# Performance work log

Hardware: AMD Instinct MI355X
Metric: run time of the kernel (lower is better)

The kernel has to match this reference:

```python
import jax, jax.numpy as jnp
import numpy as np


def conv1d(x, w, b):
    # x: (N, Cin, W), w: (Cout, Cin, K) -> (N, Cout, W-K+1), VALID conv (torch Conv1d)
    y = jax.lax.conv_general_dilated(x, w, (1,), 'VALID', dimension_numbers=('NCH', 'OIH', 'NCH'))
    return y + b[None, :, None]


def cnn_block(x, w, b):
    # conv1d then MaxPool1d over the full valid length -> (N, Cout)
    return jnp.max(conv1d(x, w, b), axis=2)


def highway(x, Wp, bp, Wg, bg):
    p = jax.nn.relu(x @ Wp.T + bp)
    g = jax.nn.sigmoid(x @ Wg.T + bg)
    return g * p + (1.0 - g) * x


def lstm_masked(x, lens, Wih, Whh, bih, bhh):
    # x: (N, Wt, E); lens: (N,) valid lengths. Emulates pack_padded_sequence +
    # nn.LSTM + pad_packed_sequence: outputs are h_t for t < len, zeros after.
    N, Wt, _ = x.shape
    H = Whh.shape[1]
    bias = bih + bhh
    h0 = jnp.zeros((N, H), x.dtype)

    def step(carry, inp):
        xt, t = inp
        h, c = carry
        z = xt @ Wih.T + h @ Whh.T + bias  # (N, 4H), gate order i,f,g,o
        i, f, g, o = jnp.split(z, 4, axis=-1)
        c2 = jax.nn.sigmoid(f) * c + jax.nn.sigmoid(i) * jnp.tanh(g)
        h2 = jax.nn.sigmoid(o) * jnp.tanh(c2)
        valid = (t < lens)[:, None]
        h2 = jnp.where(valid, h2, h)
        c2 = jnp.where(valid, c2, c)
        return (h2, c2), jnp.where(valid, h2, jnp.zeros_like(h2))

    xs = jnp.moveaxis(x, 1, 0)  # (Wt, N, E)
    ts = jnp.arange(Wt)
    _, out = jax.lax.scan(step, (h0, h0), (xs, ts))
    return jnp.moveaxis(out, 0, 1)  # (N, Wt, H)


def setup_inputs() -> dict:
    key = jax.random.key(0)
    ks = jax.random.split(key, 32)
    B, T = 32, 48
    WL, WA, WE = 33, 50, 30
    EL, EA, EE, H = 300, 988, 20, 128
    CL, CA, CE = 128, 256, 64
    s = 0.02
    inp = {
        'x_lin': jax.random.normal(ks[0], (B, T, WL, EL), jnp.float32),
        'x_aco': jax.random.normal(ks[1], (B, T, WA, EA), jnp.float32),
        'x_emo': jax.random.normal(ks[2], (B, T, WE, EE), jnp.float32),
        'window_length': jax.random.randint(ks[3], (B, T), 0, WE).astype(jnp.int32) + 1,
        'length': jax.random.randint(ks[4], (B,), 1, T + 1).astype(jnp.int32),
        # CNN params
        'convL_w': s * jax.random.normal(ks[5], (CL, EL, 5), jnp.float32),
        'convL_b': jnp.zeros((CL,), jnp.float32),
        'convA_w': s * jax.random.normal(ks[6], (CA, EA, 10), jnp.float32),
        'convA_b': jnp.zeros((CA,), jnp.float32),
        'convE_w': s * jax.random.normal(ks[7], (CE, H, 3), jnp.float32),
        'convE_b': jnp.zeros((CE,), jnp.float32),
        # Highway params
        'hwL_Wp': s * jax.random.normal(ks[8], (CL, CL), jnp.float32),
        'hwL_bp': jnp.zeros((CL,), jnp.float32),
        'hwL_Wg': s * jax.random.normal(ks[9], (CL, CL), jnp.float32),
        'hwL_bg': jnp.zeros((CL,), jnp.float32),
        'hwA_Wp': s * jax.random.normal(ks[10], (CA, CA), jnp.float32),
        'hwA_bp': jnp.zeros((CA,), jnp.float32),
        'hwA_Wg': s * jax.random.normal(ks[11], (CA, CA), jnp.float32),
        'hwA_bg': jnp.zeros((CA,), jnp.float32),
        'hwE_Wp': s * jax.random.normal(ks[12], (CE, CE), jnp.float32),
        'hwE_bp': jnp.zeros((CE,), jnp.float32),
        'hwE_Wg': s * jax.random.normal(ks[13], (CE, CE), jnp.float32),
        'hwE_bg': jnp.zeros((CE,), jnp.float32),
        # LSTM params (nn.LSTM, 1 layer, batch_first)
        'lstm_Wih': s * jax.random.normal(ks[14], (4 * H, EE), jnp.float32),
        'lstm_Whh': s * jax.random.normal(ks[15], (4 * H, H), jnp.float32),
        'lstm_bih': jnp.zeros((4 * H,), jnp.float32),
        'lstm_bhh': jnp.zeros((4 * H,), jnp.float32),
    }
    return inp


def reference(x_lin, x_aco, x_emo, window_length, length,
              convL_w, convL_b, convA_w, convA_b, convE_w, convE_b,
              hwL_Wp, hwL_bp, hwL_Wg, hwL_bg,
              hwA_Wp, hwA_bp, hwA_Wg, hwA_bg,
              hwE_Wp, hwE_bp, hwE_Wg, hwE_bg,
              lstm_Wih, lstm_Whh, lstm_bih, lstm_bhh):
    B, T = x_lin.shape[:2]
    # Linguistic: per-window CNN + Highway (dropout = identity in eval)
    xl = x_lin.reshape(B * T, x_lin.shape[2], x_lin.shape[3]).transpose(0, 2, 1)  # (BT, 300, WL)
    outL = highway(cnn_block(xl, convL_w, convL_b), hwL_Wp, hwL_bp, hwL_Wg, hwL_bg)
    outL = outL.reshape(B, T, -1)
    # Acoustic
    xa = x_aco.reshape(B * T, x_aco.shape[2], x_aco.shape[3]).transpose(0, 2, 1)  # (BT, 988, WA)
    outA = highway(cnn_block(xa, convA_w, convA_b), hwA_Wp, hwA_bp, hwA_Wg, hwA_bg)
    outA = outA.reshape(B, T, -1)
    # Emotient: ragged per-window LSTM (packed semantics) -> CNN -> Highway
    xe = x_emo.reshape(B * T, x_emo.shape[2], x_emo.shape[3])  # (BT, WE, 20)
    lens = window_length.reshape(B * T)
    h = lstm_masked(xe, lens, lstm_Wih, lstm_Whh, lstm_bih, lstm_bhh)  # (BT, WE, 128)
    outE = highway(cnn_block(h.transpose(0, 2, 1), convE_w, convE_b), hwE_Wp, hwE_bp, hwE_Wg, hwE_bg)
    outE = outE.reshape(B, T, -1)
    # Concatenate modalities -> (B, T, 128+256+64) fed to the downstream head
    return jnp.concatenate([outL, outA, outE], axis=2)
```

## Files before the change

### kernel.cpp

```cpp
#include <hip/hip_runtime.h>
#include <hip/hip_bf16.h>
#include <math.h>

#define BTOT 1536
#define EL 300
#define ELP 320
#define WL_ 33
#define CL 128
#define LOUTL 29
#define KPL 1600
#define EA 988
#define EAP 992
#define WA_ 50
#define CA 256
#define LOUTA 41
#define KPA 9920
#define EE 20
#define WE_ 30
#define HH 128
#define CE 64
#define LOUTE 28
#define KPE 384
#define KDIML 1500
#define KDIMA 9880
#define KDIME 384

typedef __attribute__((ext_vector_type(4))) float f32x4;
typedef __attribute__((ext_vector_type(8))) short short8;

__device__ __forceinline__ unsigned short f2bf(float f) {
    unsigned int x = __float_as_uint(f);
    unsigned int r = (x + 0x7fffu + ((x >> 16) & 1u)) >> 16;
    return (unsigned short)r;
}

__device__ __forceinline__ float sigmf(float x) {
    return __builtin_amdgcn_rcpf(1.f + __expf(-x));
}
__device__ __forceinline__ float tanh_fast(float x) {
    return 1.f - 2.f * __builtin_amdgcn_rcpf(1.f + __expf(2.f * x));
}

#define GLD16(gp, lp) __builtin_amdgcn_global_load_lds( \
    (const __attribute__((address_space(1))) void*)(gp), \
    (__attribute__((address_space(3))) void*)(lp), 16, 0, 0)

template<int N> __device__ __forceinline__ void vmwait() {
    if constexpr (N == 0) asm volatile("s_waitcnt vmcnt(0)" ::: "memory");
    else if constexpr (N == 1) asm volatile("s_waitcnt vmcnt(1)" ::: "memory");
    else if constexpr (N == 2) asm volatile("s_waitcnt vmcnt(2)" ::: "memory");
    else if constexpr (N == 3) asm volatile("s_waitcnt vmcnt(3)" ::: "memory");
    else if constexpr (N == 4) asm volatile("s_waitcnt vmcnt(4)" ::: "memory");
    else if constexpr (N == 5) asm volatile("s_waitcnt vmcnt(5)" ::: "memory");
    else if constexpr (N == 6) asm volatile("s_waitcnt vmcnt(6)" ::: "memory");
    else if constexpr (N == 8) asm volatile("s_waitcnt vmcnt(8)" ::: "memory");
    else static_assert(N == 0, "add case");
}

__device__ __forceinline__ void tr_one(const float* a, float* at, int R, int C, int idx) {
    int r = idx / C, c = idx - r * C;
    at[c * R + r] = a[idx];
}
template<int CIN, int CINP, int KW, int COUT, int KPAD>
__device__ __forceinline__ void wt_one(const float* w, unsigned short* wt, int idx) {
    int co = idx / KPAD;
    int p  = idx - co * KPAD;
    int k  = p / CINP;
    int c  = p - k * CINP;
    float v = 0.f;
    if (k < KW && c < CIN) v = w[(co * CIN + c) * KW + k];
    wt[idx] = f2bf(v);
}
template<bool BIG>
__global__ void prep_all(const float* hwL_Wp, float* WpTL, const float* hwL_Wg, float* WgTL,
                         const float* hwA_Wp, float* WpTA, const float* hwA_Wg, float* WgTA,
                         const float* hwE_Wp, float* WpTE, const float* hwE_Wg, float* WgTE,
                         const float* lstm_Wih, float* WihT, const float* lstm_Whh, float* WhhT,
                         const float* convL_w, unsigned short* wtL,
                         const float* convE_w, unsigned short* wtE,
                         const float* convA_w, unsigned short* wtA,
                         unsigned short* whh_bf, unsigned short* wihp_bf) {
    constexpr int S1 = 16384, S2 = 16384, S3 = 65536, S4 = 65536, S5 = 4096, S6 = 4096;
    constexpr int S7 = 512 * 20, S8 = 512 * 128;
    constexpr int S9 = 128 * KPL, S10 = 64 * KPE, S11 = 512 * 128, S12 = 512 * 32;
    constexpr int S13 = CA * KPA;
    constexpr int SMALL = S1 + S2 + S3 + S4 + S5 + S6 + S7 + S8;
    constexpr int TOTAL = BIG ? (SMALL + S9 + S10 + S11 + S12 + S13) : SMALL;
    int stride = gridDim.x * blockDim.x;
    for (int i = blockIdx.x * blockDim.x + threadIdx.x; i < TOTAL; i += stride) {
        int idx = i;
        if (idx < S1) { tr_one(hwL_Wp, WpTL, 128, 128, idx); continue; } idx -= S1;
        if (idx < S2) { tr_one(hwL_Wg, WgTL, 128, 128, idx); continue; } idx -= S2;
        if (idx < S3) { tr_one(hwA_Wp, WpTA, 256, 256, idx); continue; } idx -= S3;
        if (idx < S4) { tr_one(hwA_Wg, WgTA, 256, 256, idx); continue; } idx -= S4;
        if (idx < S5) { tr_one(hwE_Wp, WpTE, 64, 64, idx); continue; } idx -= S5;
        if (idx < S6) { tr_one(hwE_Wg, WgTE, 64, 64, idx); continue; } idx -= S6;
        if (idx < S7) { tr_one(lstm_Wih, WihT, 512, 20, idx); continue; } idx -= S7;
        if (idx < S8) { tr_one(lstm_Whh, WhhT, 512, 128, idx); continue; } idx -= S8;
        if constexpr (BIG) {
            if (idx < S9) { wt_one<EL, ELP, 5, CL, KPL>(convL_w, wtL, idx); continue; } idx -= S9;
            if (idx < S10) { wt_one<HH, HH, 3, CE, KPE>(convE_w, wtE, idx); continue; } idx -= S10;
            if (idx < S11) { whh_bf[idx] = f2bf(lstm_Whh[idx]); continue; } idx -= S11;
            if (idx < S12) { int col = idx >> 5, e = idx & 31;
                             wihp_bf[idx] = (e < 20) ? f2bf(lstm_Wih[col * 20 + e]) : (unsigned short)0;
                             continue; } idx -= S12;
            wt_one<EA, EAP, 10, CA, KPA>(convA_w, wtA, idx);
        }
    }
}

template<int CIN, int CINP>
__device__ __forceinline__ void cvt_chunk(const float* in, unsigned short* out, int idx) {
    constexpr int CH = CINP / 8;
    int row = idx / CH, c0 = (idx - row * CH) * 8;
    const float* src = in + (size_t)row * CIN + c0;
    union { short8 s; unsigned short u[8]; } o;
    if (c0 + 8 <= CIN) {
        float4 v0 = *(const float4*)src;
        float4 v1 = *(const float4*)(src + 4);
        o.u[0]=f2bf(v0.x); o.u[1]=f2bf(v0.y); o.u[2]=f2bf(v0.z); o.u[3]=f2bf(v0.w);
        o.u[4]=f2bf(v1.x); o.u[5]=f2bf(v1.y); o.u[6]=f2bf(v1.z); o.u[7]=f2bf(v1.w);
    } else {
        #pragma unroll
        for (int j = 0; j < 8; ++j) o.u[j] = (c0 + j < CIN) ? f2bf(src[j]) : (unsigned short)0;
    }
    *(short8*)(out + (size_t)row * CINP + c0) = o.s;
}

#define LSTM_BLOCKS 96
#define CVTA_BLOCKS 1440

__global__ __launch_bounds__(512, 1)
void lstm_cvt(const float* __restrict__ x_emo,
              const unsigned short* __restrict__ wihp_bf, const unsigned short* __restrict__ whh_bf,
              const float* __restrict__ bih, const float* __restrict__ bhh,
              const int* __restrict__ lens, unsigned short* __restrict__ hbuf,
              const float* __restrict__ xa, unsigned short* __restrict__ outa)
{
    __shared__ __align__(16) unsigned short xq[WE_ * 16 * 32];
    __shared__ __align__(16) char h_s[2 * 16 * HH * 2];

    if (blockIdx.x >= LSTM_BLOCKS) {
        constexpr int NAC = (BTOT * WA_) * (EAP / 8);
        int stride = CVTA_BLOCKS * 512;
        for (int i = (blockIdx.x - LSTM_BLOCKS) * 512 + threadIdx.x; i < NAC; i += stride)
            cvt_chunk<EA, EAP>(xa, outa, i);
        return;
    }

    const int tid  = threadIdx.x;
    const int w    = tid >> 6;
    const int lane = tid & 63;
    const int lr   = lane & 15;
    const int lq   = lane >> 4;
    const int s0   = blockIdx.x * 16;
    const int c    = w * 16 + lr;

    short8 bfr[4][4];
    short8 bw[4];
    float bj[4];
    #pragma unroll
    for (int g = 0; g < 4; ++g) {
        int col = g * 128 + c;
        #pragma unroll
        for (int kt = 0; kt < 4; ++kt)
            bfr[g][kt] = *(const short8*)(whh_bf + (size_t)col * 128 + kt * 32 + lq * 8);
        bw[g] = *(const short8*)(wihp_bf + (size_t)col * 32 + lq * 8);
        bj[g] = bih[col] + bhh[col];
    }
    int len4[4];
    #pragma unroll
    for (int j = 0; j < 4; ++j) len4[j] = lens[s0 + lq * 4 + j];

    for (int i = tid; i < WE_ * 16 * 32; i += 512) {
        int t = i >> 9, r = (i >> 5) & 15, e = i & 31;
        xq[i] = (e < 20) ? f2bf(x_emo[(((size_t)(s0 + r) * WE_) + t) * 20 + e]) : (unsigned short)0;
    }
    for (int i = tid; i < 2048; i += 512) ((unsigned int*)h_s)[i] = 0u;

    float c_prev[4] = {0.f, 0.f, 0.f, 0.f};
    unsigned short hb_prev[4] = {0, 0, 0, 0};
    __syncthreads();

    for (int t = 0; t < WE_; ++t) {
        const char* hsr = h_s + (t & 1) * 4096;
        char* hsw = h_s + ((t & 1) ^ 1) * 4096;
        short8 ax = *(const short8*)((const char*)xq + (size_t)(t * 16 + lr) * 64 + lq * 16);
        short8 af[4];
        #pragma unroll
        for (int kt = 0; kt < 4; ++kt)
            af[kt] = *(const short8*)(hsr + ((lr * 256 + kt * 64 + lq * 16) ^ ((lr & 7) << 4)));
        f32x4 acc[4];
        #pragma unroll
        for (int g = 0; g < 4; ++g)
            acc[g] = __builtin_amdgcn_mfma_f32_16x16x32_bf16(ax, bw[g], (f32x4){0.f,0.f,0.f,0.f}, 0, 0, 0);
        #pragma unroll
        for (int kt = 0; kt < 4; ++kt)
            #pragma unroll
            for (int g = 0; g < 4; ++g)
                acc[g] = __builtin_amdgcn_mfma_f32_16x16x32_bf16(af[kt], bfr[g][kt], acc[g], 0, 0, 0);
        #pragma unroll
        for (int j = 0; j < 4; ++j) {
            int s = lq * 4 + j;
            float zi = acc[0][j] + bj[0];
            float zf = acc[1][j] + bj[1];
            float zg = acc[2][j] + bj[2];
            float zo = acc[3][j] + bj[3];
            float si = sigmf(zi), sf = sigmf(zf), so = sigmf(zo);
            float tg = tanh_fast(zg);
            float c2 = sf * c_prev[j] + si * tg;
            float h2 = so * tanh_fast(c2);
            bool valid = (t < len4[j]);
            c_prev[j] = valid ? c2 : c_prev[j];
            unsigned short h2b = f2bf(h2);
            unsigned short hn = valid ? h2b : hb_prev[j];
            hb_prev[j] = hn;
            *(unsigned short*)(hsw + (((s * HH + c) * 2) ^ ((s & 7) << 4))) = hn;
            hbuf[(((size_t)(s0 + s) * WE_) + t) * HH + c] = valid ? h2b : (unsigned short)0;
        }
        __syncthreads();
    }
}

#define CONVA_BLOCKS 768
#define CVTL_BLOCKS 512
__global__ __launch_bounds__(256, 2)
void conv_a_v11(const unsigned short* __restrict__ xb, const unsigned short* __restrict__ wt,
                const float* __restrict__ bias, float* __restrict__ pooled,
                const float* __restrict__ xl, unsigned short* __restrict__ outl)
{
    constexpr int LOUT = LOUTA, WIN = WA_, CINP = EAP, BN = 128, COUT = CA;
    constexpr int CCH  = CINP / 32;
    constexpr int KB   = CINP * 2;
    constexpr int KTOTB = CINP * 10 * 2;
    constexpr int ABUF = 4 * 64 * 64;
    constexpr int BBUF = BN * 64;
    constexpr int CPQ  = 96;

    __shared__ __align__(16) char smem[2 * ABUF + 5 * BBUF];

    if (blockIdx.x >= CONVA_BLOCKS) {
        constexpr int NLC = (BTOT * WL_) * (ELP / 8);
        int stride = CVTL_BLOCKS * 256;
        for (int i = (blockIdx.x - CONVA_BLOCKS) * 256 + threadIdx.x; i < NLC; i += stride)
            cvt_chunk<EL, ELP>(xl, outl, i);
        return;
    }

    const int tid  = threadIdx.x;
    const int lane = tid & 63;
    const int wid  = tid >> 6;
    const int lr   = lane & 15;
    const int lq   = lane >> 4;
    const int lq16 = lq * 16;

    int xcd = blockIdx.x & 7;
    int n = xcd & 1;
    int m = (xcd >> 1) * CPQ + (blockIdx.x >> 3);

    f32x4 acc[3][8];
    #pragma unroll
    for (int i = 0; i < 3; ++i)
        #pragma unroll
        for (int j = 0; j < 8; ++j) acc[i][j] = (f32x4){0.f, 0.f, 0.f, 0.f};

    const int aw_r = tid >> 2;
    const int aw   = (aw_r < WIN) ? aw_r : (WIN - 1);
    const int slot = tid & 3;
    const char* asrc[4];
    #pragma unroll
    for (int i = 0; i < 4; ++i)
        asrc[i] = (const char*)xb + ((size_t)((m * 4 + i) * WIN + aw)) * KB
                + ((slot * 16) ^ (((aw_r >> 1) & 3) << 4));
    const char* bsrc[2];
    #pragma unroll
    for (int i = 0; i < 2; ++i) {
        int col = (tid + i * 256) >> 2;
        bsrc[i] = (const char*)wt + (size_t)(n * BN + col) * KTOTB
                + ((slot * 16) ^ (((col >> 1) & 3) << 4));
    }

    char* const abuf0 = smem;
    char* const abuf1 = smem + ABUF;
    char* const bbase = smem + 2 * ABUF;

    int cbo[8];
    #pragma unroll
    for (int nf = 0; nf < 8; ++nf) {
        int cb = nf * 16 + lr;
        cbo[nf] = cb * 64 + (lq16 ^ (((cb >> 1) & 3) << 4));
    }

    #pragma unroll
    for (int i = 0; i < 4; ++i)
        GLD16(asrc[i], abuf0 + i * 4096 + tid * 16);
    #pragma unroll
    for (int s = 0; s < 3; ++s) {
        GLD16(bsrc[0] + s * KB, bbase + s * BBUF + tid * 16);
        GLD16(bsrc[1] + s * KB, bbase + s * BBUF + 4096 + tid * 16);
    }
    vmwait<0>();
    __builtin_amdgcn_s_barrier();

    int bcur = 0;

#define VSTEP(KK, DOA, DOBAR, WN, DOBSTG, CHN) do {                                \
    const char* bb = bbase + bcur * BBUF;                                          \
    short8 afr[3];                                                                 \
    _Pragma("unroll")                                                              \
    for (int o = 0; o < 3; ++o) {                                                  \
        int row = o * 16 + lr + (KK);                                              \
        afr[o] = *(const short8*)(awave + row * 64 + (lq16 ^ (((row >> 1) & 3) << 4))); \
    }                                                                              \
    short8 bf[8];                                                                  \
    _Pragma("unroll")                                                              \
    for (int nf = 0; nf < 8; ++nf) bf[nf] = *(const short8*)(bb + cbo[nf]);        \
    if (DOBSTG) {                                                                  \
        constexpr int K3 = ((KK) + 3 < 10) ? (KK) + 3 : (KK) - 7;                  \
        int boff = K3 * KB + (CHN) * 64;                                           \
        int b3 = bcur + 3; if (b3 >= 5) b3 -= 5;                                   \
        char* bstg = bbase + b3 * BBUF;                                            \
        GLD16(bsrc[0] + boff, bstg + tid * 16);                                    \
        GLD16(bsrc[1] + boff, bstg + 4096 + tid * 16);                             \
    }                                                                              \
    if (DOA) GLD16(asrc[(KK) - 5] + (size_t)(ci + 1) * 64,                         \
                   abn + ((KK) - 5) * 4096 + tid * 16);                            \
    __builtin_amdgcn_s_setprio(1);                                                 \
    _Pragma("unroll")                                                              \
    for (int nf = 0; nf < 8; ++nf)                                                 \
        _Pragma("unroll")                                                          \
        for (int o = 0; o < 3; ++o)                                                \
            acc[o][nf] = __builtin_amdgcn_mfma_f32_16x16x32_bf16(afr[o], bf[nf], acc[o][nf], 0, 0, 0); \
    __builtin_amdgcn_s_setprio(0);                                                 \
    if (DOBAR) { vmwait<WN>(); asm volatile("" ::: "memory");                      \
                 __builtin_amdgcn_s_barrier(); }                                   \
    bcur = (bcur == 4) ? 0 : bcur + 1;                                             \
} while (0)

    for (int ci = 0; ci < CCH - 1; ++ci) {
        const char* ab = (ci & 1) ? abuf1 : abuf0;
        char* abn = (ci & 1) ? abuf0 : abuf1;
        const char* awave = ab + wid * 4096;
        VSTEP(0, false, false, 0, true, ci);
        VSTEP(1, false, true,  2, true, ci);
        VSTEP(2, false, false, 0, true, ci);
        VSTEP(3, false, true,  2, true, ci);
        VSTEP(4, false, false, 0, true, ci);
        VSTEP(5, true,  true,  3, true, ci);
        VSTEP(6, true,  false, 0, true, ci);
        VSTEP(7, true,  true,  3, true, ci + 1);
        VSTEP(8, true,  false, 0, true, ci + 1);
        VSTEP(9, false, true,  2, true, ci + 1);
    }
    {
        const int ci = CCH - 1;
        const char* ab = (ci & 1) ? abuf1 : abuf0;
        char* abn = (ci & 1) ? abuf0 : abuf1; (void)abn;
        const char* awave = ab + wid * 4096;
        VSTEP(0, false, false, 0, true,  ci);
        VSTEP(1, false, true,  2, true,  ci);
        VSTEP(2, false, false, 0, true,  ci);
        VSTEP(3, false, true,  2, true,  ci);
        VSTEP(4, false, false, 0, true,  ci);
        VSTEP(5, false, true,  2, true,  ci);
        VSTEP(6, false, false, 0, true,  ci);
        VSTEP(7, false, true,  0, false, ci);
        VSTEP(8, false, false, 0, false, ci);
        VSTEP(9, false, true,  0, false, ci);
    }
#undef VSTEP

    const int bt = m * 4 + wid;
    #pragma unroll
    for (int nf = 0; nf < 8; ++nf) {
        float mx = -INFINITY;
        #pragma unroll
        for (int o = 0; o < 3; ++o) {
            int rb = o * 16 + lq * 4;
            #pragma unroll
            for (int j = 0; j < 4; ++j)
                if (rb + j < LOUT) mx = fmaxf(mx, acc[o][nf][j]);
        }
        mx = fmaxf(mx, __shfl_xor(mx, 16, 64));
        mx = fmaxf(mx, __shfl_xor(mx, 32, 64));
        if (lane < 16) {
            int col = n * BN + nf * 16 + lane;
            pooled[(size_t)bt * COUT + col] = mx + bias[col];
        }
    }
}

template<int LOUT, int WIN, int CINP, int KW, int BN, int NS, int MFR, int COUT>
__global__ __launch_bounds__(256, 2)
void conv_pool_v10(const unsigned short* __restrict__ xb, const unsigned short* __restrict__ wt,
                   const float* __restrict__ bias, float* __restrict__ pooled)
{
    constexpr int CCH   = CINP / 32;
    constexpr int KB    = CINP * 2;
    constexpr int KTOTB = CINP * KW * 2;
    constexpr int NFR   = BN / 16;
    constexpr int B_IT  = BN / 64;
    constexpr int ABUF  = 4 * 64 * 64;
    constexpr int BBUF  = BN * 64;
    constexpr int CPQ   = (BTOT / 4) / 4;

    __shared__ __align__(16) char smem[2 * ABUF + 4 * BBUF];

    const int tid  = threadIdx.x;
    const int lane = tid & 63;
    const int wid  = tid >> 6;
    const int lr   = lane & 15;
    const int lq   = lane >> 4;
    const int lq16 = lq * 16;

    int m, n;
    if constexpr (NS == 2) {
        int xcd = blockIdx.x & 7;
        n = xcd & 1;
        m = (xcd >> 1) * CPQ + (blockIdx.x >> 3);
    } else {
        m = blockIdx.x; n = 0;
    }

    f32x4 acc[MFR][NFR];
    #pragma unroll
    for (int i = 0; i < MFR; ++i)
        #pragma unroll
        for (int j = 0; j < NFR; ++j) acc[i][j] = (f32x4){0.f, 0.f, 0.f, 0.f};

    const int aw_r = tid >> 2;
    const int aw   = (aw_r < WIN) ? aw_r : (WIN - 1);
    const int slot = tid & 3;
    const char* asrc[4];
    #pragma unroll
    for (int i = 0; i < 4; ++i)
        asrc[i] = (const char*)xb + ((size_t)((m * 4 + i) * WIN + aw)) * KB
                + ((slot * 16) ^ (((aw_r >> 1) & 3) << 4));
    const char* bsrc[B_IT];
    #pragma unroll
    for (int i = 0; i < B_IT; ++i) {
        int col = (tid + i * 256) >> 2;
        bsrc[i] = (const char*)wt + (size_t)(n * BN + col) * KTOTB
                + ((slot * 16) ^ (((col >> 1) & 3) << 4));
    }

    char* const abuf0 = smem;
    char* const abuf1 = smem + ABUF;
    char* const bbase = smem + 2 * ABUF;

    int cbo[NFR];
    #pragma unroll
    for (int nf = 0; nf < NFR; ++nf) {
        int cb = nf * 16 + lr;
        cbo[nf] = cb * 64 + (lq16 ^ (((cb >> 1) & 3) << 4));
    }

    #pragma unroll
    for (int i = 0; i < 4; ++i)
        GLD16(asrc[i], abuf0 + i * 4096 + tid * 16);
    #pragma unroll
    for (int s = 0; s < 3; ++s)
        #pragma unroll
        for (int i = 0; i < B_IT; ++i)
            GLD16(bsrc[i] + s * KB, bbase + s * BBUF + i * 4096 + tid * 16);
    vmwait<0>();
    __builtin_amdgcn_s_barrier();

    int bcur = 0;

#define STEP(KK, WN, TAIL) do {                                                    \
    const char* bb = bbase + bcur * BBUF;                                          \
    short8 afr[MFR];                                                               \
    _Pragma("unroll")                                                              \
    for (int o = 0; o < MFR; ++o) {                                                \
        int row = o * 16 + lr + (KK);                                              \
        afr[o] = *(const short8*)(awave + row * 64 + (lq16 ^ (((row >> 1) & 3) << 4))); \
    }                                                                              \
    short8 bf[NFR];                                                                \
    _Pragma("unroll")                                                              \
    for (int nf = 0; nf < NFR; ++nf) bf[nf] = *(const short8*)(bb + cbo[nf]);      \
    if (!(TAIL) || (KK) < KW - 3) {                                                \
        constexpr int k3_ = ((KK) + 3 < KW) ? (KK) + 3 : (KK) + 3 - KW;            \
        int boff = k3_ * KB + (((KK) + 3 < KW) ? ci : ci + 1) * 64;                \
        char* bstg = bbase + ((bcur + 3) & 3) * BBUF;                              \
        _Pragma("unroll")                                                          \
        for (int i = 0; i < B_IT; ++i)                                             \
            GLD16(bsrc[i] + boff, bstg + i * 4096 + tid * 16);                     \
    }                                                                              \
    if (!(TAIL)) {                                                                 \
        if (KW >= 8) {                                                             \
            if ((KK) < 4)                                                          \
                GLD16(asrc[(KK) & 3] + (size_t)(ci + 1) * 64, abn + ((KK) & 3) * 4096 + tid * 16); \
        } else if ((KK) == 0) {                                                    \
            _Pragma("unroll")                                                      \
            for (int i = 0; i < 4; ++i)                                            \
                GLD16(asrc[i] + (size_t)(ci + 1) * 64, abn + i * 4096 + tid * 16); \
        }                                                                          \
    }                                                                              \
    __builtin_amdgcn_s_setprio(1);                                                 \
    _Pragma("unroll")                                                              \
    for (int nf = 0; nf < NFR; ++nf)                                               \
        _Pragma("unroll")                                                          \
        for (int o = 0; o < MFR; ++o)                                              \
            acc[o][nf] = __builtin_amdgcn_mfma_f32_16x16x32_bf16(afr[o], bf[nf], acc[o][nf], 0, 0, 0); \
    __builtin_amdgcn_s_setprio(0);                                                 \
    vmwait<WN>();                                                                  \
    asm volatile("" ::: "memory");                                                 \
    __builtin_amdgcn_s_barrier();                                                  \
    bcur = (bcur + 1) & 3;                                                         \
} while (0)

    for (int ci = 0; ci < CCH - 1; ++ci) {
        const char* ab = (ci & 1) ? abuf1 : abuf0;
        char* abn = (ci & 1) ? abuf0 : abuf1;
        const char* awave = ab + wid * 4096;
        if constexpr (KW == 5) {
            STEP(0, 8, false); STEP(1, 8, false); STEP(2, 4, false); STEP(3, 4, false); STEP(4, 4, false);
        } else {
            STEP(0, 6, false); STEP(1, 6, false); STEP(2, 2, false);
        }
    }
    {
        const int ci = CCH - 1;
        const char* ab = (ci & 1) ? abuf1 : abuf0;
        char* abn = (ci & 1) ? abuf0 : abuf1; (void)abn;
        const char* awave = ab + wid * 4096;
        if constexpr (KW == 5) {
            STEP(0, 4, true); STEP(1, 4, true); STEP(2, 2, true); STEP(3, 0, true); STEP(4, 0, true);
        } else {
            STEP(0, 1, true); STEP(1, 0, true); STEP(2, 0, true);
        }
    }
#undef STEP

    const int bt = m * 4 + wid;
    #pragma unroll
    for (int nf = 0; nf < NFR; ++nf) {
        float mx = -INFINITY;
        #pragma unroll
        for (int o = 0; o < MFR; ++o) {
            int rb = o * 16 + lq * 4;
            #pragma unroll
            for (int j = 0; j < 4; ++j)
                if (rb + j < LOUT) mx = fmaxf(mx, acc[o][nf][j]);
        }
        mx = fmaxf(mx, __shfl_xor(mx, 16, 64));
        mx = fmaxf(mx, __shfl_xor(mx, 32, 64));
        if (lane < 16) {
            int col = n * BN + nf * 16 + lane;
            pooled[(size_t)bt * COUT + col] = mx + bias[col];
        }
    }
}

#define HWA_BLOCKS 192
#define HWL_BLOCKS 96
#define HWE_BLOCKS 48
__global__ __launch_bounds__(256)
void highway_v2(const float* __restrict__ pL, const float* __restrict__ pA, const float* __restrict__ pE,
                const float* __restrict__ WpTL, const float* __restrict__ bpL,
                const float* __restrict__ WgTL, const float* __restrict__ bgL,
                const float* __restrict__ WpTA, const float* __restrict__ bpA,
                const float* __restrict__ WgTA, const float* __restrict__ bgA,
                const float* __restrict__ WpTE, const float* __restrict__ bpE,
                const float* __restrict__ WgTE, const float* __restrict__ bgE,
                float* __restrict__ out) {
    __shared__ float xs[2048];
    int bx = blockIdx.x;
    int tid = threadIdx.x;
    if (bx < HWA_BLOCKS) {
        int bt0 = bx * 8;
        #pragma unroll
        for (int s = 0; s < 8; ++s) xs[s * 256 + tid] = pA[(size_t)(bt0 + s) * 256 + tid];
        __syncthreads();
        float p[8], g[8];
        #pragma unroll
        for (int s = 0; s < 8; ++s) { p[s] = bpA[tid]; g[s] = bgA[tid]; }
        for (int c = 0; c < 256; ++c) {
            float wp = WpTA[c * 256 + tid], wg = WgTA[c * 256 + tid];
            #pragma unroll
            for (int s = 0; s < 8; ++s) {
                float xv = xs[s * 256 + c];
                p[s] += xv * wp; g[s] += xv * wg;
            }
        }
        #pragma unroll
        for (int s = 0; s < 8; ++s) {
            float pp = fmaxf(p[s], 0.f);
            float gg = sigmf(g[s]);
            out[(size_t)(bt0 + s) * 448 + 128 + tid] = gg * pp + (1.f - gg) * xs[s * 256 + tid];
        }
    } else if (bx < HWA_BLOCKS + HWL_BLOCKS) {
        int bt0 = (bx - HWA_BLOCKS) * 16;
        for (int i = tid; i < 16 * 128; i += 256) xs[i] = pL[(size_t)bt0 * 128 + i];
        __syncthreads();
        int j = tid & 127, h = tid >> 7;
        float p[8], g[8];
        #pragma unroll
        for (int s = 0; s < 8; ++s) { p[s] = bpL[j]; g[s] = bgL[j]; }
        for (int c = 0; c < 128; ++c) {
            float wp = WpTL[c * 128 + j], wg = WgTL[c * 128 + j];
            #pragma unroll
            for (int s = 0; s < 8; ++s) {
                float xv = xs[(h * 8 + s) * 128 + c];
                p[s] += xv * wp; g[s] += xv * wg;
            }
        }
        #pragma unroll
        for (int s = 0; s < 8; ++s) {
            float pp = fmaxf(p[s], 0.f);
            float gg = sigmf(g[s]);
            out[(size_t)(bt0 + h * 8 + s) * 448 + j] = gg * pp + (1.f - gg) * xs[(h * 8 + s) * 128 + j];
        }
    } else {
        int bt0 = (bx - HWA_BLOCKS - HWL_BLOCKS) * 32;
        for (int i = tid; i < 32 * 64; i += 256) xs[i] = pE[(size_t)bt0 * 64 + i];
        __syncthreads();
        int j = tid & 63, grp = tid >> 6;
        float p[8], g[8];
        #pragma unroll
        for (int s = 0; s < 8; ++s) { p[s] = bpE[j]; g[s] = bgE[j]; }
        for (int c = 0; c < 64; ++c) {
            float wp = WpTE[c * 64 + j], wg = WgTE[c * 64 + j];
            #pragma unroll
            for (int s = 0; s < 8; ++s) {
                float xv = xs[(grp * 8 + s) * 64 + c];
                p[s] += xv * wp; g[s] += xv * wg;
            }
        }
        #pragma unroll
        for (int s = 0; s < 8; ++s) {
            float pp = fmaxf(p[s], 0.f);
            float gg = sigmf(g[s]);
            out[(size_t)(bt0 + grp * 8 + s) * 448 + 384 + j] = gg * pp + (1.f - gg) * xs[(grp * 8 + s) * 64 + j];
        }
    }
}

__global__ __launch_bounds__(512)
void lstm_kernel_f32(const float* __restrict__ x, const int* __restrict__ lens,
                     const float* __restrict__ WihT, const float* __restrict__ WhhT,
                     const float* __restrict__ bih, const float* __restrict__ bhh,
                     float* __restrict__ hout) {
    int bt = blockIdx.x;
    int j  = threadIdx.x;
    __shared__ float xs[WE_][EE];
    __shared__ __align__(16) float hs[HH];
    __shared__ float zs[512];
    for (int idx = j; idx < WE_ * EE; idx += 512)
        ((float*)xs)[idx] = x[(size_t)bt * WE_ * EE + idx];
    if (j < HH) hs[j] = 0.f;
    float wih[EE];
    #pragma unroll
    for (int e = 0; e < EE; ++e) wih[e] = WihT[e * 512 + j];
    float whh[HH];
    #pragma unroll
    for (int h = 0; h < HH; ++h) whh[h] = WhhT[h * 512 + j];
    float bjv = bih[j] + bhh[j];
    float c_reg = 0.f;
    int len = lens[bt];
    __syncthreads();
    for (int t = 0; t < WE_; ++t) {
        float z = bjv;
        #pragma unroll
        for (int e = 0; e < EE; ++e) z += wih[e] * xs[t][e];
        const float4* h4 = (const float4*)hs;
        #pragma unroll
        for (int q = 0; q < HH / 4; ++q) {
            float4 hv = h4[q];
            z += whh[4*q+0] * hv.x + whh[4*q+1] * hv.y
               + whh[4*q+2] * hv.z + whh[4*q+3] * hv.w;
        }
        zs[j] = z;
        __syncthreads();
        if (j < HH) {
            float zi = zs[j], zf = zs[HH + j], zg = zs[2*HH + j], zo = zs[3*HH + j];
            float si = 1.f / (1.f + expf(-zi));
            float sf = 1.f / (1.f + expf(-zf));
            float so = 1.f / (1.f + expf(-zo));
            float tg = tanhf(zg);
            float c2 = sf * c_reg + si * tg;
            float h2 = so * tanhf(c2);
            bool valid = (t < len);
            float hn = valid ? h2 : hs[j];
            c_reg    = valid ? c2 : c_reg;
            hout[((size_t)bt * WE_ + t) * HH + j] = valid ? h2 : 0.f;
            hs[j] = hn;
        }
        __syncthreads();
    }
}

template<int CIN, int WIN, int COUT, int KDIM, int LOUT>
__global__ __launch_bounds__(256)
void conv_pool_simple(const float* __restrict__ x, const float* __restrict__ w,
                      const float* __restrict__ bias, float* __restrict__ pooled)
{
    constexpr int KW = KDIM / CIN;
    int bt = blockIdx.x;
    int co = blockIdx.y * 64 + (threadIdx.x & 63);
    int seg = threadIdx.x >> 6;
    __shared__ float part[4][64];
    float m = -INFINITY;
    for (int l = seg; l < LOUT; l += 4) {
        float acc = 0.f;
        for (int k = 0; k < KW; ++k) {
            const float* xr = x + ((size_t)bt * WIN + l + k) * CIN;
            const float* wr = w + ((size_t)co * CIN) * KW + k;
            for (int cc = 0; cc < CIN; ++cc) acc += xr[cc] * wr[(size_t)cc * KW];
        }
        m = fmaxf(m, acc);
    }
    part[seg][threadIdx.x & 63] = m;
    __syncthreads();
    if (threadIdx.x < 64) {
        float mm = fmaxf(fmaxf(part[0][threadIdx.x], part[1][threadIdx.x]),
                         fmaxf(part[2][threadIdx.x], part[3][threadIdx.x]));
        pooled[(size_t)bt * COUT + co] = mm + bias[co];
    }
}

static inline int cdiv(int a, int b) { return (a + b - 1) / b; }

extern "C" void kernel_launch(void* const* d_in, const int* in_sizes, int n_in,
                              void* d_out, int out_size, void* d_ws, size_t ws_size,
                              hipStream_t stream) {
    const float* x_lin  = (const float*)d_in[0];
    const float* x_aco  = (const float*)d_in[1];
    const float* x_emo  = (const float*)d_in[2];
    const int*   wlen   = (const int*)  d_in[3];
    const float* convL_w = (const float*)d_in[5];
    const float* convL_b = (const float*)d_in[6];
    const float* convA_w = (const float*)d_in[7];
    const float* convA_b = (const float*)d_in[8];
    const float* convE_w = (const float*)d_in[9];
    const float* convE_b = (const float*)d_in[10];
    const float* hwL_Wp = (const float*)d_in[11];
    const float* hwL_bp = (const float*)d_in[12];
    const float* hwL_Wg = (const float*)d_in[13];
    const float* hwL_bg = (const float*)d_in[14];
    const float* hwA_Wp = (const float*)d_in[15];
    const float* hwA_bp = (const float*)d_in[16];
    const float* hwA_Wg = (const float*)d_in[17];
    const float* hwA_bg = (const float*)d_in[18];
    const float* hwE_Wp = (const float*)d_in[19];
    const float* hwE_bp = (const float*)d_in[20];
    const float* hwE_Wg = (const float*)d_in[21];
    const float* hwE_bg = (const float*)d_in[22];
    const float* lstm_Wih = (const float*)d_in[23];
    const float* lstm_Whh = (const float*)d_in[24];
    const float* lstm_bih = (const float*)d_in[25];
    const float* lstm_bhh = (const float*)d_in[26];
    float* out = (float*)d_out;

    char* p0 = (char*)d_ws;
    char* p = p0;
    auto alloc = [&](size_t bytes) { char* r = p; p += (bytes + 255) & ~(size_t)255; return r; };
    float* WpTL = (float*)alloc((size_t)CL * CL * 4);
    float* WgTL = (float*)alloc((size_t)CL * CL * 4);
    float* WpTA = (float*)alloc((size_t)CA * CA * 4);
    float* WgTA = (float*)alloc((size_t)CA * CA * 4);
    float* WpTE = (float*)alloc((size_t)CE * CE * 4);
    float* WgTE = (float*)alloc((size_t)CE * CE * 4);
    float* WihT = (float*)alloc((size_t)EE * 512 * 4);
    float* WhhT = (float*)alloc((size_t)HH * 512 * 4);
    unsigned short* whh_bf  = (unsigned short*)alloc((size_t)512 * 128 * 2);
    unsigned short* wihp_bf = (unsigned short*)alloc((size_t)512 * 32 * 2);
    void*  hbuf = (void*)alloc((size_t)BTOT * WE_ * HH * 4);
    float* pL   = (float*)alloc((size_t)BTOT * CL * 4);
    float* pA   = (float*)alloc((size_t)BTOT * CA * 4);
    float* pE   = (float*)alloc((size_t)BTOT * CE * 4);
    unsigned short* wtA = (unsigned short*)alloc((size_t)CA * KPA * 2);
    unsigned short* wtL = (unsigned short*)alloc((size_t)CL * KPL * 2);
    unsigned short* wtE = (unsigned short*)alloc((size_t)CE * KPE * 2);
    unsigned short* xlin_p = (unsigned short*)alloc((size_t)BTOT * WL_ * ELP * 2 + 64);
    unsigned short* xaco_p = (unsigned short*)alloc((size_t)BTOT * WA_ * EAP * 2 + 64);
    size_t need = (size_t)(p - p0);
    bool big = ws_size >= need;

    if (big) {
        prep_all<true><<<2048, 256, 0, stream>>>(hwL_Wp, WpTL, hwL_Wg, WgTL, hwA_Wp, WpTA, hwA_Wg, WgTA,
                                                 hwE_Wp, WpTE, hwE_Wg, WgTE, lstm_Wih, WihT, lstm_Whh, WhhT,
                                                 convL_w, wtL, convE_w, wtE, convA_w, wtA, whh_bf, wihp_bf);
        lstm_cvt<<<LSTM_BLOCKS + CVTA_BLOCKS, 512, 0, stream>>>(
            x_emo, wihp_bf, whh_bf, lstm_bih, lstm_bhh, wlen, (unsigned short*)hbuf,
            x_aco, xaco_p);
        conv_a_v11<<<CONVA_BLOCKS + CVTL_BLOCKS, 256, 0, stream>>>(
            xaco_p, wtA, convA_b, pA, x_lin, xlin_p);
        conv_pool_v10<LOUTL, WL_, ELP, 5, 128, 1, 2, CL>
            <<<384, 256, 0, stream>>>(xlin_p, wtL, convL_b, pL);
        conv_pool_v10<LOUTE, WE_, HH, 3, 64, 1, 2, CE>
            <<<384, 256, 0, stream>>>((const unsigned short*)hbuf, wtE, convE_b, pE);
        highway_v2<<<HWA_BLOCKS + HWL_BLOCKS + HWE_BLOCKS, 256, 0, stream>>>(
            pL, pA, pE, WpTL, hwL_bp, WgTL, hwL_bg, WpTA, hwA_bp, WgTA, hwA_bg,
            WpTE, hwE_bp, WgTE, hwE_bg, out);
    } else {
        prep_all<false><<<2048, 256, 0, stream>>>(hwL_Wp, WpTL, hwL_Wg, WgTL, hwA_Wp, WpTA, hwA_Wg, WgTA,
                                                  hwE_Wp, WpTE, hwE_Wg, WgTE, lstm_Wih, WihT, lstm_Whh, WhhT,
                                                  convL_w, wtL, convE_w, wtE, convA_w, wtA, whh_bf, wihp_bf);
        lstm_kernel_f32<<<BTOT, 512, 0, stream>>>(x_emo, wlen, WihT, WhhT, lstm_bih, lstm_bhh, (float*)hbuf);
        conv_pool_simple<EA, WA_, CA, KDIMA, LOUTA>
            <<<dim3(BTOT, CA / 64), 256, 0, stream>>>(x_aco, convA_w, convA_b, pA);
        conv_pool_simple<EL, WL_, CL, KDIML, LOUTL>
            <<<dim3(BTOT, CL / 64), 256, 0, stream>>>(x_lin, convL_w, convL_b, pL);
        conv_pool_simple<HH, WE_, CE, KDIME, LOUTE>
            <<<dim3(BTOT, CE / 64), 256, 0, stream>>>((const float*)hbuf, convE_w, convE_b, pE);
        highway_v2<<<HWA_BLOCKS + HWL_BLOCKS + HWE_BLOCKS, 256, 0, stream>>>(
            pL, pA, pE, WpTL, hwL_bp, WgTL, hwL_bg, WpTA, hwA_bp, WgTA, hwA_bg,
            WpTE, hwE_bp, WgTE, hwE_bg, out);
    }
}
```

Baseline: 518.6 us.

## Enlarge acoustic conv tile to 12 windows per block and merge input conversions

The acoustic conv kernel now runs 768-thread blocks covering 12 windows each, so every staged weight tile is reused by 12 waves instead of 4. Only 8 waves stage B, and the B ring shrinks from 5 to 4 buffers with a barrier on every step. The linguistic fp32-to-bf16 conversion moves out of the conv launch and into the LSTM/convert launch, which leaves the conv kernel purely compute. Costs: a larger LDS footprint (about 128KB per block), more frequent barriers, and the conversion work now sharing a launch with the LSTM.

Result: slower. 869.8 us (+67.7%).

```diff
diff --git a/kernel.cpp b/kernel.cpp
--- a/kernel.cpp
+++ b/kernel.cpp
@@ -128,23 +128,27 @@
 }
 
 #define LSTM_BLOCKS 96
-#define CVTA_BLOCKS 1440
+#define CVT_BLOCKS 1952
 
 __global__ __launch_bounds__(512, 1)
 void lstm_cvt(const float* __restrict__ x_emo,
               const unsigned short* __restrict__ wihp_bf, const unsigned short* __restrict__ whh_bf,
               const float* __restrict__ bih, const float* __restrict__ bhh,
               const int* __restrict__ lens, unsigned short* __restrict__ hbuf,
-              const float* __restrict__ xa, unsigned short* __restrict__ outa)
+              const float* __restrict__ xa, const float* __restrict__ xl,
+              unsigned short* __restrict__ outa, unsigned short* __restrict__ outl)
 {
     __shared__ __align__(16) unsigned short xq[WE_ * 16 * 32];
     __shared__ __align__(16) char h_s[2 * 16 * HH * 2];
 
     if (blockIdx.x >= LSTM_BLOCKS) {
         constexpr int NAC = (BTOT * WA_) * (EAP / 8);
-        int stride = CVTA_BLOCKS * 512;
-        for (int i = (blockIdx.x - LSTM_BLOCKS) * 512 + threadIdx.x; i < NAC; i += stride)
-            cvt_chunk<EA, EAP>(xa, outa, i);
+        constexpr int NLC = (BTOT * WL_) * (ELP / 8);
+        int stride = CVT_BLOCKS * 512;
+        for (int i = (blockIdx.x - LSTM_BLOCKS) * 512 + threadIdx.x; i < NAC + NLC; i += stride) {
+            if (i < NAC) cvt_chunk<EA, EAP>(xa, outa, i);
+            else         cvt_chunk<EL, ELP>(xl, outl, i - NAC);
+        }
         return;
     }
 
@@ -222,30 +226,19 @@
     }
 }
 
-#define CONVA_BLOCKS 768
-#define CVTL_BLOCKS 512
-__global__ __launch_bounds__(256, 2)
-void conv_a_v11(const unsigned short* __restrict__ xb, const unsigned short* __restrict__ wt,
-                const float* __restrict__ bias, float* __restrict__ pooled,
-                const float* __restrict__ xl, unsigned short* __restrict__ outl)
+#define CONVA12_BLOCKS 256
+__global__ __launch_bounds__(768, 3)
+void conv_a12(const unsigned short* __restrict__ xb, const unsigned short* __restrict__ wt,
+              const float* __restrict__ bias, float* __restrict__ pooled)
 {
-    constexpr int LOUT = LOUTA, WIN = WA_, CINP = EAP, BN = 128, COUT = CA;
+    constexpr int CINP = EAP, BN = 128, COUT = CA, KW = 10, LOUT = LOUTA, WIN = WA_;
     constexpr int CCH  = CINP / 32;
     constexpr int KB   = CINP * 2;
-    constexpr int KTOTB = CINP * 10 * 2;
-    constexpr int ABUF = 4 * 64 * 64;
+    constexpr int KTOTB = CINP * KW * 2;
+    constexpr int ABUF = 12 * 4096;
     constexpr int BBUF = BN * 64;
-    constexpr int CPQ  = 96;
-
-    __shared__ __align__(16) char smem[2 * ABUF + 5 * BBUF];
-
-    if (blockIdx.x >= CONVA_BLOCKS) {
-        constexpr int NLC = (BTOT * WL_) * (ELP / 8);
-        int stride = CVTL_BLOCKS * 256;
-        for (int i = (blockIdx.x - CONVA_BLOCKS) * 256 + threadIdx.x; i < NLC; i += stride)
-            cvt_chunk<EL, ELP>(xl, outl, i);
-        return;
-    }
+
+    __shared__ __align__(16) char smem[2 * ABUF + 4 * BBUF];
 
     const int tid  = threadIdx.x;
     const int lane = tid & 63;
@@ -253,10 +246,11 @@
     const int lr   = lane & 15;
     const int lq   = lane >> 4;
     const int lq16 = lq * 16;
+    const bool bstager = (wid < 8);
 
     int xcd = blockIdx.x & 7;
     int n = xcd & 1;
-    int m = (xcd >> 1) * CPQ + (blockIdx.x >> 3);
+    int m = (xcd >> 1) * 32 + (blockIdx.x >> 3);
 
     f32x4 acc[3][8];
     #pragma unroll
@@ -264,21 +258,18 @@
         #pragma unroll
         for (int j = 0; j < 8; ++j) acc[i][j] = (f32x4){0.f, 0.f, 0.f, 0.f};
 
-    const int aw_r = tid >> 2;
-    const int aw   = (aw_r < WIN) ? aw_r : (WIN - 1);
-    const int slot = tid & 3;
     const char* asrc[4];
     #pragma unroll
-    for (int i = 0; i < 4; ++i)
-        asrc[i] = (const char*)xb + ((size_t)((m * 4 + i) * WIN + aw)) * KB
-                + ((slot * 16) ^ (((aw_r >> 1) & 3) << 4));
-    const char* bsrc[2];
-    #pragma unroll
-    for (int i = 0; i < 2; ++i) {
-        int col = (tid + i * 256) >> 2;
-        bsrc[i] = (const char*)wt + (size_t)(n * BN + col) * KTOTB
-                + ((slot * 16) ^ (((col >> 1) & 3) << 4));
-    }
+    for (int i = 0; i < 4; ++i) {
+        int c = tid + i * 768;
+        int s = c >> 8, r = (c >> 2) & 63, slot = c & 3;
+        int rv = (r < WIN) ? r : (WIN - 1);
+        asrc[i] = (const char*)xb + ((size_t)((m * 12 + s) * WIN + rv)) * KB
+                + ((slot * 16) ^ (((r >> 1) & 3) << 4));
+    }
+    const char* bsrc = (const char*)wt
+        + (size_t)(n * BN + (tid >> 2)) * KTOTB
+        + (((tid & 3) * 16) ^ ((((tid >> 2) >> 1) & 3) << 4));
 
     char* const abuf0 = smem;
     char* const abuf1 = smem + ABUF;
@@ -293,18 +284,18 @@
 
     #pragma unroll
     for (int i = 0; i < 4; ++i)
-        GLD16(asrc[i], abuf0 + i * 4096 + tid * 16);
-    #pragma unroll
-    for (int s = 0; s < 3; ++s) {
-        GLD16(bsrc[0] + s * KB, bbase + s * BBUF + tid * 16);
-        GLD16(bsrc[1] + s * KB, bbase + s * BBUF + 4096 + tid * 16);
+        GLD16(asrc[i], abuf0 + (tid + i * 768) * 16);
+    if (bstager) {
+        #pragma unroll
+        for (int s = 0; s < 3; ++s)
+            GLD16(bsrc + s * KB, bbase + s * BBUF + tid * 16);
     }
     vmwait<0>();
     __builtin_amdgcn_s_barrier();
 
     int bcur = 0;
 
-#define VSTEP(KK, DOA, DOBAR, WN, DOBSTG, CHN) do {                                \
+#define STEP(KK, W07, W811, TAIL) do {                                             \
     const char* bb = bbase + bcur * BBUF;                                          \
     short8 afr[3];                                                                 \
     _Pragma("unroll")                                                              \
@@ -315,16 +306,13 @@
     short8 bf[8];                                                                  \
     _Pragma("unroll")                                                              \
     for (int nf = 0; nf < 8; ++nf) bf[nf] = *(const short8*)(bb + cbo[nf]);        \
-    if (DOBSTG) {                                                                  \
-        constexpr int K3 = ((KK) + 3 < 10) ? (KK) + 3 : (KK) - 7;                  \
-        int boff = K3 * KB + (CHN) * 64;                                           \
-        int b3 = bcur + 3; if (b3 >= 5) b3 -= 5;                                   \
-        char* bstg = bbase + b3 * BBUF;                                            \
-        GLD16(bsrc[0] + boff, bstg + tid * 16);                                    \
-        GLD16(bsrc[1] + boff, bstg + 4096 + tid * 16);                             \
+    if ((!(TAIL) || (KK) < KW - 3) && bstager) {                \
+        constexpr int K3 = ((KK) + 3 < KW) ? (KK) + 3 : (KK) + 3 - KW;             \
+        int boff = K3 * KB + (((KK) + 3 < KW) ? ci : ci + 1) * 64;                 \
+        GLD16(bsrc + boff, bbase + ((bcur + 3) & 3) * BBUF + tid * 16);            \
     }                                                                              \
-    if (DOA) GLD16(asrc[(KK) - 5] + (size_t)(ci + 1) * 64,                         \
-                   abn + ((KK) - 5) * 4096 + tid * 16);                            \
+    if (!(TAIL) && (KK) < 4)                  \
+        GLD16(asrc[KK] + (size_t)(ci + 1) * 64, abn + (tid + (KK) * 768) * 16);    \
     __builtin_amdgcn_s_setprio(1);                                                 \
     _Pragma("unroll")                                                              \
     for (int nf = 0; nf < 8; ++nf)                                                 \
@@ -332,45 +320,34 @@
         for (int o = 0; o < 3; ++o)                                                \
             acc[o][nf] = __builtin_amdgcn_mfma_f32_16x16x32_bf16(afr[o], bf[nf], acc[o][nf], 0, 0, 0); \
     __builtin_amdgcn_s_setprio(0);                                                 \
-    if (DOBAR) { vmwait<WN>(); asm volatile("" ::: "memory");                      \
-                 __builtin_amdgcn_s_barrier(); }                                   \
-    bcur = (bcur == 4) ? 0 : bcur + 1;                                             \
+    if (bstager) vmwait<W07>(); else vmwait<W811>();                               \
+    asm volatile("" ::: "memory");                                                 \
+    __builtin_amdgcn_s_barrier();                                                  \
+    bcur = (bcur + 1) & 3;                                                         \
 } while (0)
 
     for (int ci = 0; ci < CCH - 1; ++ci) {
         const char* ab = (ci & 1) ? abuf1 : abuf0;
         char* abn = (ci & 1) ? abuf0 : abuf1;
         const char* awave = ab + wid * 4096;
-        VSTEP(0, false, false, 0, true, ci);
-        VSTEP(1, false, true,  2, true, ci);
-        VSTEP(2, false, false, 0, true, ci);
-        VSTEP(3, false, true,  2, true, ci);
-        VSTEP(4, false, false, 0, true, ci);
-        VSTEP(5, true,  true,  3, true, ci);
-        VSTEP(6, true,  false, 0, true, ci);
-        VSTEP(7, true,  true,  3, true, ci + 1);
-        VSTEP(8, true,  false, 0, true, ci + 1);
-        VSTEP(9, false, true,  2, true, ci + 1);
+        STEP(0, 3, 1, false); STEP(1, 4, 2, false); STEP(2, 4, 2, false);
+        STEP(3, 4, 2, false); STEP(4, 3, 1, false); STEP(5, 2, 0, false);
+        STEP(6, 2, 0, false); STEP(7, 2, 0, false); STEP(8, 2, 0, false);
+        STEP(9, 2, 0, false);
     }
     {
         const int ci = CCH - 1;
         const char* ab = (ci & 1) ? abuf1 : abuf0;
         char* abn = (ci & 1) ? abuf0 : abuf1; (void)abn;
         const char* awave = ab + wid * 4096;
-        VSTEP(0, false, false, 0, true,  ci);
-        VSTEP(1, false, true,  2, true,  ci);
-        VSTEP(2, false, false, 0, true,  ci);
-        VSTEP(3, false, true,  2, true,  ci);
-        VSTEP(4, false, false, 0, true,  ci);
-        VSTEP(5, false, true,  2, true,  ci);
-        VSTEP(6, false, false, 0, true,  ci);
-        VSTEP(7, false, true,  0, false, ci);
-        VSTEP(8, false, false, 0, false, ci);
-        VSTEP(9, false, true,  0, false, ci);
-    }
-#undef VSTEP
-
-    const int bt = m * 4 + wid;
+        STEP(0, 2, 0, true); STEP(1, 2, 0, true); STEP(2, 2, 0, true);
+        STEP(3, 2, 0, true); STEP(4, 2, 0, true); STEP(5, 2, 0, true);
+        STEP(6, 2, 0, true); STEP(7, 1, 0, true); STEP(8, 0, 0, true);
+        STEP(9, 0, 0, true);
+    }
+#undef STEP
+
+    const int bt = m * 12 + wid;
     #pragma unroll
     for (int nf = 0; nf < 8; ++nf) {
         float mx = -INFINITY;
@@ -782,11 +759,10 @@
         prep_all<true><<<2048, 256, 0, stream>>>(hwL_Wp, WpTL, hwL_Wg, WgTL, hwA_Wp, WpTA, hwA_Wg, WgTA,
                                                  hwE_Wp, WpTE, hwE_Wg, WgTE, lstm_Wih, WihT, lstm_Whh, WhhT,
                                                  convL_w, wtL, convE_w, wtE, convA_w, wtA, whh_bf, wihp_bf);
-        lstm_cvt<<<LSTM_BLOCKS + CVTA_BLOCKS, 512, 0, stream>>>(
+        lstm_cvt<<<LSTM_BLOCKS + CVT_BLOCKS, 512, 0, stream>>>(
             x_emo, wihp_bf, whh_bf, lstm_bih, lstm_bhh, wlen, (unsigned short*)hbuf,
-            x_aco, xaco_p);
-        conv_a_v11<<<CONVA_BLOCKS + CVTL_BLOCKS, 256, 0, stream>>>(
-            xaco_p, wtA, convA_b, pA, x_lin, xlin_p);
+            x_aco, x_lin, xaco_p, xlin_p);
+        conv_a12<<<CONVA12_BLOCKS, 768, 0, stream>>>(xaco_p, wtA, convA_b, pA);
         conv_pool_v10<LOUTL, WL_, ELP, 5, 128, 1, 2, CL>
             <<<384, 256, 0, stream>>>(xlin_p, wtL, convL_b, pL);
         conv_pool_v10<LOUTE, WE_, HH, 3, 64, 1, 2, CE>
```
